# Performance work log

Hardware: AMD Instinct MI355X
Metric: run time of the kernel (lower is better)

## Reference

```python
import jax, jax.numpy as jnp
import numpy as np

B, T, D_MEM, D_Q, D_ATT, C_LOC, K = 64, 2000, 512, 1024, 128, 32, 31


def setup_inputs() -> dict:
    key = jax.random.key(0)
    ks = jax.random.split(key, 9)
    return {
        "attention_hidden_state": jax.random.normal(ks[0], (B, 1, D_Q), jnp.float32),
        "memory": jax.random.normal(ks[1], (B, T, D_MEM), jnp.float32),
        "processed_memory": jax.random.normal(ks[2], (B, T, D_ATT), jnp.float32),
        "attention_weights": jax.random.uniform(ks[3], (B, 2, T), jnp.float32),
        "Wq": jax.random.normal(ks[4], (D_Q, D_ATT), jnp.float32) * 0.02,
        "Wconv": jax.random.normal(ks[5], (C_LOC, 2, K), jnp.float32) * 0.1,
        "bconv": jax.random.normal(ks[6], (C_LOC,), jnp.float32) * 0.01,
        "Wloc": jax.random.normal(ks[7], (C_LOC, D_ATT), jnp.float32) * 0.1,
        "v": jax.random.normal(ks[8], (D_ATT,), jnp.float32) * 0.1,
    }


def reference(attention_hidden_state, memory, processed_memory, attention_weights,
              Wq, Wconv, bconv, Wloc, v):
    # query projection: [B,1,1024] @ [1024,128] -> [B,1,128]
    processed_query = jnp.einsum("bqi,io->bqo", attention_hidden_state, Wq)
    # location conv: [B,2,T] -> [B,32,T], 'same' padding (k=31, pad=15)
    loc = jax.lax.conv_general_dilated(
        attention_weights, Wconv, window_strides=(1,), padding=[(15, 15)],
        dimension_numbers=("NCH", "OIH", "NCH"))
    loc = loc + bconv[None, :, None]
    # transpose to [B,T,32] then project to [B,T,128]
    processed_loc = jnp.einsum("bct,co->bto", loc, Wloc)
    # energies: v . tanh(q + loc + mem) -> [B,T]
    energies = jnp.einsum("btd,d->bt", jnp.tanh(processed_query + processed_loc + processed_memory), v)
    new_weights = jax.nn.softmax(energies, axis=1)
    # context: [B,T] x [B,T,D] -> [B,D]
    attention_context = jnp.einsum("bt,btd->bd", new_weights, memory)
    return attention_context, new_weights
```

## Files before the change

kernel.cpp:

```cpp
#include <hip/hip_runtime.h>

#define B 64
#define T 2000
#define D_MEM 512
#define D_Q 1024
#define D_ATT 128
#define C_LOC 32
#define K 31

#define CH2 100
#define NCH2 (T / CH2)
#define CH3 50
#define NPART (T / CH3)

#define WS_PQ    0
#define WS_EXPW  (WS_PQ + B * D_ATT)
#define WS_SUMS  (WS_EXPW + B * T)
#define WS_PART  (WS_SUMS + B * NCH2)

__device__ __forceinline__ float tanh_fast(float x) {
    float e = __expf(2.f * x);
    return 1.f - 2.f / (e + 1.f);
}

__global__ __launch_bounds__(512) void pq_kernel(const float* __restrict__ h,
                                                 const float* __restrict__ Wq,
                                                 float* __restrict__ pq) {
    int b = blockIdx.x;
    int tid = threadIdx.x;
    int ty = tid >> 7;
    int d  = tid & 127;
    __shared__ float sh[D_Q];
    __shared__ float red[4][D_ATT];
    const float* hb = h + (size_t)b * D_Q;
    if (tid < D_Q / 4) ((float4*)sh)[tid] = ((const float4*)hb)[tid];
    __syncthreads();
    float acc = 0.f;
    int ibeg = ty * 256;
#pragma unroll 8
    for (int i2 = 0; i2 < 256; ++i2) {
        int i = ibeg + i2;
        acc = fmaf(sh[i], Wq[(size_t)i * D_ATT + d], acc);
    }
    red[ty][d] = acc;
    __syncthreads();
    if (ty == 0)
        pq[b * D_ATT + d] = red[0][d] + red[1][d] + red[2][d] + red[3][d];
}

#define EFIN(PL, PM, ROW)                                                    \
    {                                                                        \
        float e = vv.x * tanh_fast(pqv.x + (PL).x + (PM).x)                  \
                + vv.y * tanh_fast(pqv.y + (PL).y + (PM).y)                  \
                + vv.z * tanh_fast(pqv.z + (PL).z + (PM).z)                  \
                + vv.w * tanh_fast(pqv.w + (PL).w + (PM).w);                 \
        e += __shfl_xor(e, 16); e += __shfl_xor(e, 8);                       \
        e += __shfl_xor(e, 4);  e += __shfl_xor(e, 2);                       \
        e += __shfl_xor(e, 1);                                               \
        if (dd == 0) s_e[ROW] = __expf(e);                                   \
    }

__global__ __launch_bounds__(256, 4) void energy_kernel(
    const float* __restrict__ aw, const float* __restrict__ pmem,
    const float* __restrict__ pq, const float* __restrict__ Wconv,
    const float* __restrict__ bconv, const float* __restrict__ Wloc,
    const float* __restrict__ v, float* __restrict__ expw,
    float* __restrict__ sums) {
    const int s = blockIdx.x, b = blockIdx.y;
    const int t0 = s * CH2;
    const int tid = threadIdx.x;

    __shared__ float s_aw[2][CH2 + K - 1];
    __shared__ float s_wc[2 * K * C_LOC];
    __shared__ float s_loc[104][C_LOC];
    __shared__ float s_wloc[C_LOC * D_ATT];
    __shared__ float s_pq[D_ATT];
    __shared__ float s_e[CH2];
    __shared__ float s_red[2];

    const int AWW = CH2 + K - 1;
    for (int j = tid; j < 2 * AWW; j += 256) {
        int i = j / AWW, o = j - i * AWW;
        int t = t0 - (K / 2) + o;
        s_aw[i][o] = (t >= 0 && t < T) ? aw[((size_t)b * 2 + i) * T + t] : 0.f;
    }
    for (int j = tid; j < C_LOC * 2 * K; j += 256) {
        int c = j / (2 * K), r = j - c * 2 * K;
        int i = r / K, k = r - i * K;
        s_wc[(i * K + k) * C_LOC + c] = Wconv[j];
    }
    for (int j = tid; j < C_LOC * D_ATT / 4; j += 256)
        ((float4*)s_wloc)[j] = ((const float4*)Wloc)[j];
    if (tid < D_ATT) s_pq[tid] = pq[b * D_ATT + tid];
    __syncthreads();

    {
        int g = tid >> 5, c = tid & 31;
        float bc = bconv[c];
        float a0 = bc, a1 = bc, a2 = bc, a3 = bc, a4 = bc, a5 = bc, a6 = bc,
              a7 = bc, a8 = bc, a9 = bc, a10 = bc, a11 = bc, a12 = bc;
        for (int i = 0; i < 2; ++i) {
#pragma unroll 4
            for (int k = 0; k < K; ++k) {
                float wv = s_wc[(i * K + k) * C_LOC + c];
                const float* sa = &s_aw[i][g + k];
                a0  = fmaf(sa[0],  wv, a0);
                a1  = fmaf(sa[8],  wv, a1);
                a2  = fmaf(sa[16], wv, a2);
                a3  = fmaf(sa[24], wv, a3);
                a4  = fmaf(sa[32], wv, a4);
                a5  = fmaf(sa[40], wv, a5);
                a6  = fmaf(sa[48], wv, a6);
                a7  = fmaf(sa[56], wv, a7);
                a8  = fmaf(sa[64], wv, a8);
                a9  = fmaf(sa[72], wv, a9);
                a10 = fmaf(sa[80], wv, a10);
                a11 = fmaf(sa[88], wv, a11);
                a12 = fmaf(sa[96], wv, a12);
            }
        }
        s_loc[g +  0][c] = a0;  s_loc[g +  8][c] = a1;
        s_loc[g + 16][c] = a2;  s_loc[g + 24][c] = a3;
        s_loc[g + 32][c] = a4;  s_loc[g + 40][c] = a5;
        s_loc[g + 48][c] = a6;  s_loc[g + 56][c] = a7;
        s_loc[g + 64][c] = a8;  s_loc[g + 72][c] = a9;
        s_loc[g + 80][c] = a10; s_loc[g + 88][c] = a11;
        s_loc[g + 96][c] = a12;
    }
    __syncthreads();

    {
        int g = tid >> 5, dd = tid & 31;
        float4 pqv = ((const float4*)s_pq)[dd];
        float4 vv  = ((const float4*)v)[dd];
        const float4* pmb =
            (const float4*)(pmem + ((size_t)b * T + t0) * D_ATT);

        for (int jc = 0; jc < 3; ++jc) {
            int r0 = g + 32 * jc;
            float4 pm0 = pmb[(size_t)(r0)      * (D_ATT / 4) + dd];
            float4 pm1 = pmb[(size_t)(r0 +  8) * (D_ATT / 4) + dd];
            float4 pm2 = pmb[(size_t)(r0 + 16) * (D_ATT / 4) + dd];
            float4 pm3 = pmb[(size_t)(r0 + 24) * (D_ATT / 4) + dd];
            float4 pl0 = make_float4(0.f, 0.f, 0.f, 0.f);
            float4 pl1 = make_float4(0.f, 0.f, 0.f, 0.f);
            float4 pl2 = make_float4(0.f, 0.f, 0.f, 0.f);
            float4 pl3 = make_float4(0.f, 0.f, 0.f, 0.f);
#pragma unroll 4
            for (int c = 0; c < C_LOC; ++c) {
                float4 w = ((const float4*)s_wloc)[c * (D_ATT / 4) + dd];
                float l0 = s_loc[r0][c];
                float l1 = s_loc[r0 + 8][c];
                float l2 = s_loc[r0 + 16][c];
                float l3 = s_loc[r0 + 24][c];
                pl0.x = fmaf(l0, w.x, pl0.x); pl0.y = fmaf(l0, w.y, pl0.y);
                pl0.z = fmaf(l0, w.z, pl0.z); pl0.w = fmaf(l0, w.w, pl0.w);
                pl1.x = fmaf(l1, w.x, pl1.x); pl1.y = fmaf(l1, w.y, pl1.y);
                pl1.z = fmaf(l1, w.z, pl1.z); pl1.w = fmaf(l1, w.w, pl1.w);
                pl2.x = fmaf(l2, w.x, pl2.x); pl2.y = fmaf(l2, w.y, pl2.y);
                pl2.z = fmaf(l2, w.z, pl2.z); pl2.w = fmaf(l2, w.w, pl2.w);
                pl3.x = fmaf(l3, w.x, pl3.x); pl3.y = fmaf(l3, w.y, pl3.y);
                pl3.z = fmaf(l3, w.z, pl3.z); pl3.w = fmaf(l3, w.w, pl3.w);
            }
            EFIN(pl0, pm0, r0);
            EFIN(pl1, pm1, r0 + 8);
            EFIN(pl2, pm2, r0 + 16);
            EFIN(pl3, pm3, r0 + 24);
        }

        {
            int tl = g + 96;
            if (tl < CH2) {
                float4 pm = pmb[(size_t)tl * (D_ATT / 4) + dd];
                float4 pl = make_float4(0.f, 0.f, 0.f, 0.f);
#pragma unroll 4
                for (int c = 0; c < C_LOC; ++c) {
                    float4 w = ((const float4*)s_wloc)[c * (D_ATT / 4) + dd];
                    float l = s_loc[tl][c];
                    pl.x = fmaf(l, w.x, pl.x);
                    pl.y = fmaf(l, w.y, pl.y);
                    pl.z = fmaf(l, w.z, pl.z);
                    pl.w = fmaf(l, w.w, pl.w);
                }
                EFIN(pl, pm, tl);
            }
        }
    }
    __syncthreads();

    if (tid < 128) {
        float vsum = (tid < CH2) ? s_e[tid] : 0.f;
        if (tid < CH2) expw[(size_t)b * T + t0 + tid] = vsum;
        float r = vsum;
#pragma unroll
        for (int off = 32; off >= 1; off >>= 1) r += __shfl_xor(r, off);
        if ((tid & 63) == 0) s_red[tid >> 6] = r;
    }
    __syncthreads();
    if (tid == 0) sums[b * NCH2 + s] = s_red[0] + s_red[1];
}

__global__ __launch_bounds__(128, 4) void ctx_kernel(
    const float* __restrict__ expw, const float* __restrict__ sums,
    const float* __restrict__ memory, float* __restrict__ partial,
    float* __restrict__ out_w) {
    const int p = blockIdx.x, b = blockIdx.y;
    const int t0 = p * CH3;
    const int tid = threadIdx.x;
    __shared__ float s_w[CH3];
    __shared__ float s_inv;
    if (tid < 64) {
        float r = (tid < NCH2) ? sums[b * NCH2 + tid] : 0.f;
#pragma unroll
        for (int off = 32; off >= 1; off >>= 1) r += __shfl_xor(r, off);
        if (tid == 0) s_inv = 1.f / r;
    }
    if (tid < CH3) s_w[tid] = expw[(size_t)b * T + t0 + tid];
    __syncthreads();
    if (tid < CH3) out_w[(size_t)b * T + t0 + tid] = s_w[tid] * s_inv;

    const float4* mem4 = (const float4*)(memory + ((size_t)b * T + t0) * D_MEM);
    float4 acc = {0.f, 0.f, 0.f, 0.f};
#pragma unroll 10
    for (int j = 0; j < CH3; ++j) {
        float wt = s_w[j];
        float4 mv = mem4[(size_t)j * (D_MEM / 4) + tid];
        acc.x = fmaf(wt, mv.x, acc.x);
        acc.y = fmaf(wt, mv.y, acc.y);
        acc.z = fmaf(wt, mv.z, acc.z);
        acc.w = fmaf(wt, mv.w, acc.w);
    }
    ((float4*)(partial + ((size_t)p * B + b) * D_MEM))[tid] = acc;
}

__global__ __launch_bounds__(128) void finalize_kernel(
    const float* __restrict__ sums, const float* __restrict__ partial,
    float* __restrict__ out_ctx) {
    int b = blockIdx.x, tid = threadIdx.x;
    __shared__ float s_inv;
    if (tid < 64) {
        float r = (tid < NCH2) ? sums[b * NCH2 + tid] : 0.f;
#pragma unroll
        for (int off = 32; off >= 1; off >>= 1) r += __shfl_xor(r, off);
        if (tid == 0) s_inv = 1.f / r;
    }
    __syncthreads();
    float inv = s_inv;
    const float4* p4 = (const float4*)partial;
    float4 acc = {0.f, 0.f, 0.f, 0.f};
#pragma unroll
    for (int p = 0; p < NPART; ++p) {
        float4 pv = p4[((size_t)p * B + b) * (D_MEM / 4) + tid];
        acc.x += pv.x; acc.y += pv.y; acc.z += pv.z; acc.w += pv.w;
    }
    acc.x *= inv; acc.y *= inv; acc.z *= inv; acc.w *= inv;
    ((float4*)(out_ctx + (size_t)b * D_MEM))[tid] = acc;
}

extern "C" void kernel_launch(void* const* d_in, const int* in_sizes, int n_in,
                              void* d_out, int out_size, void* d_ws, size_t ws_size,
                              hipStream_t stream) {
    const float* hidden = (const float*)d_in[0];
    const float* memory = (const float*)d_in[1];
    const float* pmem   = (const float*)d_in[2];
    const float* aw     = (const float*)d_in[3];
    const float* Wq     = (const float*)d_in[4];
    const float* Wconv  = (const float*)d_in[5];
    const float* bconv  = (const float*)d_in[6];
    const float* Wloc   = (const float*)d_in[7];
    const float* v      = (const float*)d_in[8];

    float* out_ctx = (float*)d_out;
    float* out_w   = (float*)d_out + B * D_MEM;

    float* ws      = (float*)d_ws;
    float* pqp     = ws + WS_PQ;
    float* expw    = ws + WS_EXPW;
    float* sums    = ws + WS_SUMS;
    float* partial = ws + WS_PART;

    pq_kernel<<<B, 512, 0, stream>>>(hidden, Wq, pqp);
    energy_kernel<<<dim3(NCH2, B), 256, 0, stream>>>(aw, pmem, pqp, Wconv,
                                                     bconv, Wloc, v, expw, sums);
    ctx_kernel<<<dim3(NPART, B), 128, 0, stream>>>(expw, sums, memory, partial,
                                                   out_w);
    finalize_kernel<<<B, 128, 0, stream>>>(sums, partial, out_ctx);
}
```

Baseline: 455.0 us.

## Vectorize location conv and projection LDS reads with float4 register blocking

Restructures the location convolution so each thread computes 4 consecutive time steps from float4 reads of the padded attention weights and per-channel padded conv weights, reusing loaded values across taps. The Wloc projection now reads s_loc as float4 across 4 channels at a time, cutting scalar LDS loads. ctx_kernel launch bounds raise min blocks per SM from 4 to 8 to favour occupancy. Register pressure rises from the full unrolls, and the padded weight layout adds zero taps that must stay correct.

```diff
diff --git a/kernel.cpp b/kernel.cpp
--- a/kernel.cpp
+++ b/kernel.cpp
@@ -12,6 +12,7 @@
 #define NCH2 (T / CH2)
 #define CH3 50
 #define NPART (T / CH3)
+#define AWW 132
 
 #define WS_PQ    0
 #define WS_EXPW  (WS_PQ + B * D_ATT)
@@ -60,6 +61,16 @@
         if (dd == 0) s_e[ROW] = __expf(e);                                   \
     }
 
+#define PROJ4(PL, L)                                                          \
+    (PL).x = fmaf((L).x, w0.x, (PL).x); (PL).y = fmaf((L).x, w0.y, (PL).y);   \
+    (PL).z = fmaf((L).x, w0.z, (PL).z); (PL).w = fmaf((L).x, w0.w, (PL).w);   \
+    (PL).x = fmaf((L).y, w1.x, (PL).x); (PL).y = fmaf((L).y, w1.y, (PL).y);   \
+    (PL).z = fmaf((L).y, w1.z, (PL).z); (PL).w = fmaf((L).y, w1.w, (PL).w);   \
+    (PL).x = fmaf((L).z, w2.x, (PL).x); (PL).y = fmaf((L).z, w2.y, (PL).y);   \
+    (PL).z = fmaf((L).z, w2.z, (PL).z); (PL).w = fmaf((L).z, w2.w, (PL).w);   \
+    (PL).x = fmaf((L).w, w3.x, (PL).x); (PL).y = fmaf((L).w, w3.y, (PL).y);   \
+    (PL).z = fmaf((L).w, w3.z, (PL).z); (PL).w = fmaf((L).w, w3.w, (PL).w);
+
 __global__ __launch_bounds__(256, 4) void energy_kernel(
     const float* __restrict__ aw, const float* __restrict__ pmem,
     const float* __restrict__ pq, const float* __restrict__ Wconv,
@@ -70,24 +81,28 @@
     const int t0 = s * CH2;
     const int tid = threadIdx.x;
 
-    __shared__ float s_aw[2][CH2 + K - 1];
-    __shared__ float s_wc[2 * K * C_LOC];
-    __shared__ float s_loc[104][C_LOC];
+    __shared__ float s_aw[2][AWW];
+    __shared__ float s_wc2[C_LOC * 68];
+    __shared__ float s_loc[CH2][C_LOC];
     __shared__ float s_wloc[C_LOC * D_ATT];
     __shared__ float s_pq[D_ATT];
     __shared__ float s_e[CH2];
     __shared__ float s_red[2];
 
-    const int AWW = CH2 + K - 1;
     for (int j = tid; j < 2 * AWW; j += 256) {
         int i = j / AWW, o = j - i * AWW;
         int t = t0 - (K / 2) + o;
-        s_aw[i][o] = (t >= 0 && t < T) ? aw[((size_t)b * 2 + i) * T + t] : 0.f;
+        s_aw[i][o] = (o < 130 && t >= 0 && t < T)
+                         ? aw[((size_t)b * 2 + i) * T + t] : 0.f;
     }
     for (int j = tid; j < C_LOC * 2 * K; j += 256) {
         int c = j / (2 * K), r = j - c * 2 * K;
         int i = r / K, k = r - i * K;
-        s_wc[(i * K + k) * C_LOC + c] = Wconv[j];
+        s_wc2[c * 68 + i * 32 + k] = Wconv[j];
+    }
+    if (tid < C_LOC) {
+        s_wc2[tid * 68 + 31] = 0.f;
+        s_wc2[tid * 68 + 63] = 0.f;
     }
     for (int j = tid; j < C_LOC * D_ATT / 4; j += 256)
         ((float4*)s_wloc)[j] = ((const float4*)Wloc)[j];
@@ -97,35 +112,48 @@
     {
         int g = tid >> 5, c = tid & 31;
         float bc = bconv[c];
-        float a0 = bc, a1 = bc, a2 = bc, a3 = bc, a4 = bc, a5 = bc, a6 = bc,
-              a7 = bc, a8 = bc, a9 = bc, a10 = bc, a11 = bc, a12 = bc;
-        for (int i = 0; i < 2; ++i) {
-#pragma unroll 4
-            for (int k = 0; k < K; ++k) {
-                float wv = s_wc[(i * K + k) * C_LOC + c];
-                const float* sa = &s_aw[i][g + k];
-                a0  = fmaf(sa[0],  wv, a0);
-                a1  = fmaf(sa[8],  wv, a1);
-                a2  = fmaf(sa[16], wv, a2);
-                a3  = fmaf(sa[24], wv, a3);
-                a4  = fmaf(sa[32], wv, a4);
-                a5  = fmaf(sa[40], wv, a5);
-                a6  = fmaf(sa[48], wv, a6);
-                a7  = fmaf(sa[56], wv, a7);
-                a8  = fmaf(sa[64], wv, a8);
-                a9  = fmaf(sa[72], wv, a9);
-                a10 = fmaf(sa[80], wv, a10);
-                a11 = fmaf(sa[88], wv, a11);
-                a12 = fmaf(sa[96], wv, a12);
+        const float4* wc4 = (const float4*)&s_wc2[c * 68];
+#pragma unroll
+        for (int p = 0; p < 4; ++p) {
+            int q = g + 8 * p;
+            if (q <= 24) {
+                int r = 4 * q;
+                float a0 = bc, a1 = bc, a2 = bc, a3 = bc;
+#pragma unroll
+                for (int i = 0; i < 2; ++i) {
+                    const float4* aw4 = (const float4*)&s_aw[i][0];
+                    float4 A = aw4[q];
+#pragma unroll
+                    for (int kq = 0; kq < 8; ++kq) {
+                        float4 Bq = aw4[q + kq + 1];
+                        float4 wv = wc4[i * 8 + kq];
+                        a0 = fmaf(A.x, wv.x, a0);
+                        a1 = fmaf(A.y, wv.x, a1);
+                        a2 = fmaf(A.z, wv.x, a2);
+                        a3 = fmaf(A.w, wv.x, a3);
+                        a0 = fmaf(A.y, wv.y, a0);
+                        a1 = fmaf(A.z, wv.y, a1);
+                        a2 = fmaf(A.w, wv.y, a2);
+                        a3 = fmaf(Bq.x, wv.y, a3);
+                        a0 = fmaf(A.z, wv.z, a0);
+                        a1 = fmaf(A.w, wv.z, a1);
+                        a2 = fmaf(Bq.x, wv.z, a2);
+                        a3 = fmaf(Bq.y, wv.z, a3);
+                        if (kq < 7) {
+                            a0 = fmaf(A.w, wv.w, a0);
+                            a1 = fmaf(Bq.x, wv.w, a1);
+                            a2 = fmaf(Bq.y, wv.w, a2);
+                            a3 = fmaf(Bq.z, wv.w, a3);
+                        }
+                        A = Bq;
+                    }
+                }
+                s_loc[r + 0][c] = a0;
+                s_loc[r + 1][c] = a1;
+                s_loc[r + 2][c] = a2;
+                s_loc[r + 3][c] = a3;
             }
         }
-        s_loc[g +  0][c] = a0;  s_loc[g +  8][c] = a1;
-        s_loc[g + 16][c] = a2;  s_loc[g + 24][c] = a3;
-        s_loc[g + 32][c] = a4;  s_loc[g + 40][c] = a5;
-        s_loc[g + 48][c] = a6;  s_loc[g + 56][c] = a7;
-        s_loc[g + 64][c] = a8;  s_loc[g + 72][c] = a9;
-        s_loc[g + 80][c] = a10; s_loc[g + 88][c] = a11;
-        s_loc[g + 96][c] = a12;
     }
     __syncthreads();
 
@@ -135,6 +163,8 @@
         float4 vv  = ((const float4*)v)[dd];
         const float4* pmb =
             (const float4*)(pmem + ((size_t)b * T + t0) * D_ATT);
+        const float4* wl4 = (const float4*)s_wloc;
+        const float4* lc4 = (const float4*)&s_loc[0][0];
 
         for (int jc = 0; jc < 3; ++jc) {
             int r0 = g + 32 * jc;
@@ -146,21 +176,20 @@
             float4 pl1 = make_float4(0.f, 0.f, 0.f, 0.f);
             float4 pl2 = make_float4(0.f, 0.f, 0.f, 0.f);
             float4 pl3 = make_float4(0.f, 0.f, 0.f, 0.f);
-#pragma unroll 4
-            for (int c = 0; c < C_LOC; ++c) {
-                float4 w = ((const float4*)s_wloc)[c * (D_ATT / 4) + dd];
-                float l0 = s_loc[r0][c];
-                float l1 = s_loc[r0 + 8][c];
-                float l2 = s_loc[r0 + 16][c];
-                float l3 = s_loc[r0 + 24][c];
-                pl0.x = fmaf(l0, w.x, pl0.x); pl0.y = fmaf(l0, w.y, pl0.y);
-                pl0.z = fmaf(l0, w.z, pl0.z); pl0.w = fmaf(l0, w.w, pl0.w);
-                pl1.x = fmaf(l1, w.x, pl1.x); pl1.y = fmaf(l1, w.y, pl1.y);
-                pl1.z = fmaf(l1, w.z, pl1.z); pl1.w = fmaf(l1, w.w, pl1.w);
-                pl2.x = fmaf(l2, w.x, pl2.x); pl2.y = fmaf(l2, w.y, pl2.y);
-                pl2.z = fmaf(l2, w.z, pl2.z); pl2.w = fmaf(l2, w.w, pl2.w);
-                pl3.x = fmaf(l3, w.x, pl3.x); pl3.y = fmaf(l3, w.y, pl3.y);
-                pl3.z = fmaf(l3, w.z, pl3.z); pl3.w = fmaf(l3, w.w, pl3.w);
+#pragma unroll
+            for (int cq = 0; cq < 8; ++cq) {
+                float4 w0 = wl4[(4 * cq + 0) * (D_ATT / 4) + dd];
+                float4 w1 = wl4[(4 * cq + 1) * (D_ATT / 4) + dd];
+                float4 w2 = wl4[(4 * cq + 2) * (D_ATT / 4) + dd];
+                float4 w3 = wl4[(4 * cq + 3) * (D_ATT / 4) + dd];
+                float4 l0 = lc4[(size_t)(r0)      * (C_LOC / 4) + cq];
+                float4 l1 = lc4[(size_t)(r0 +  8) * (C_LOC / 4) + cq];
+                float4 l2 = lc4[(size_t)(r0 + 16) * (C_LOC / 4) + cq];
+                float4 l3 = lc4[(size_t)(r0 + 24) * (C_LOC / 4) + cq];
+                PROJ4(pl0, l0);
+                PROJ4(pl1, l1);
+                PROJ4(pl2, l2);
+                PROJ4(pl3, l3);
             }
             EFIN(pl0, pm0, r0);
             EFIN(pl1, pm1, r0 + 8);
@@ -173,14 +202,14 @@
             if (tl < CH2) {
                 float4 pm = pmb[(size_t)tl * (D_ATT / 4) + dd];
                 float4 pl = make_float4(0.f, 0.f, 0.f, 0.f);
-#pragma unroll 4
-                for (int c = 0; c < C_LOC; ++c) {
-                    float4 w = ((const float4*)s_wloc)[c * (D_ATT / 4) + dd];
-                    float l = s_loc[tl][c];
-                    pl.x = fmaf(l, w.x, pl.x);
-                    pl.y = fmaf(l, w.y, pl.y);
-                    pl.z = fmaf(l, w.z, pl.z);
-                    pl.w = fmaf(l, w.w, pl.w);
+#pragma unroll
+                for (int cq = 0; cq < 8; ++cq) {
+                    float4 w0 = wl4[(4 * cq + 0) * (D_ATT / 4) + dd];
+                    float4 w1 = wl4[(4 * cq + 1) * (D_ATT / 4) + dd];
+                    float4 w2 = wl4[(4 * cq + 2) * (D_ATT / 4) + dd];
+                    float4 w3 = wl4[(4 * cq + 3) * (D_ATT / 4) + dd];
+                    float4 l0 = lc4[(size_t)tl * (C_LOC / 4) + cq];
+                    PROJ4(pl, l0);
                 }
                 EFIN(pl, pm, tl);
             }
@@ -200,7 +229,7 @@
     if (tid == 0) sums[b * NCH2 + s] = s_red[0] + s_red[1];
 }
 
-__global__ __launch_bounds__(128, 4) void ctx_kernel(
+__global__ __launch_bounds__(128, 8) void ctx_kernel(
     const float* __restrict__ expw, const float* __restrict__ sums,
     const float* __restrict__ memory, float* __restrict__ partial,
     float* __restrict__ out_w) {
```

New measurement: 785.2 us. 1.73x slower.
